# Kernel tuning notes

Hardware: AMD Instinct MI355X
Metric: run time of the kernel (lower is better)

## Reference

```python
import jax, jax.numpy as jnp
import numpy as np

B, S, H, T = 32, 1024, 1024, 256
WINDOW = 2
ITERATIONS = 3


def setup_inputs() -> dict:
    key = jax.random.key(0)
    k1, k2, k3, k4, k5, k6 = jax.random.split(key, 6)
    token_feats = jax.random.normal(k1, (B, S, H), dtype=jnp.float32)
    unary_score = jax.random.normal(k2, (B, S, T), dtype=jnp.float32)
    lengths = jax.random.randint(k3, (B,), S // 2, S + 1)  # in [S/2, S]
    mask = (jnp.arange(S)[None, :] < lengths[:, None]).astype(jnp.float32)
    transitions = jax.random.normal(k4, (WINDOW, T, T), dtype=jnp.float32)
    start_transitions = jax.random.normal(k5, (WINDOW, T), dtype=jnp.float32)
    end_transitions = jax.random.normal(k6, (WINDOW, T), dtype=jnp.float32)
    return {
        "token_feats": token_feats,
        "unary_score": unary_score,
        "mask": mask,
        "transitions": transitions,
        "start_transitions": start_transitions,
        "end_transitions": end_transitions,
        "lengths": lengths,
    }


def reference(token_feats, unary_score, mask, transitions, start_transitions,
              end_transitions, lengths):
    # mask unary (and token_feats, as in original; token_feats is unused in
    # the plain-transitions second-order path)
    unary = unary_score * mask[..., None]        # [B,S,T]
    _ = token_feats * mask[..., None]
    q = unary
    batch_range = jnp.arange(q.shape[0])
    for _it in range(ITERATIONS):
        q = jax.nn.softmax(q, axis=-1)
        left_sum = jnp.zeros_like(q)
        right_sum = jnp.zeros_like(q)
        for j in range(1, WINDOW + 1):
            # message from left neighbor at distance j
            left_sum = left_sum.at[:, j:].add(
                jnp.einsum('nsa,ab->nsb', q[:, :-j], transitions[j - 1]))
            # message from right neighbor at distance j
            right_sum = right_sum.at[:, :-j].add(
                jnp.einsum('nsb,ab->nsa', q[:, j:], transitions[j - 1]))
            # end transitions scatter-add at position lengths - j
            right_sum = right_sum.at[batch_range, lengths - j].add(
                end_transitions[j - 1])
        msg = left_sum + right_sum
        # start transitions on first WINDOW positions (broadcast over batch)
        msg = msg.at[:, 0:WINDOW].add(start_transitions)
        q = unary + msg
        q = q * mask[..., None]
    return q
```

## Files before the change

### kernel.cpp

```cpp
#include <hip/hip_runtime.h>
#include <hip/hip_bf16.h>
#include <cstdint>


typedef __attribute__((ext_vector_type(4))) float f32x4;
typedef __attribute__((ext_vector_type(8))) short bf16x8;

__device__ __forceinline__ void load_lds16(const void* g, void* l) {
    __builtin_amdgcn_global_load_lds(
        (const __attribute__((address_space(1))) void*)g,
        (__attribute__((address_space(3))) void*)l, 16, 0, 0);
}

__device__ __forceinline__ void wct_one(const float* __restrict__ trans,
                                        __hip_bfloat16* __restrict__ wct, int e) {
    int n = e >> 10, k = e & 1023;
    int r = k >> 8, kk = k & 255;
    float v;
    if (r == 0)      v = trans[kk * 256 + n];
    else if (r == 1) v = trans[65536 + kk * 256 + n];
    else if (r == 2) v = trans[n * 256 + kk];
    else             v = trans[65536 + n * 256 + kk];
    wct[n * 1024 + k] = __float2bfloat16(v);
}

__device__ __forceinline__ void guard_one(__hip_bfloat16* Pa, __hip_bfloat16* Pb, int g) {
    __hip_bfloat16* P = (g & 32768) ? Pb : Pa;
    int rem = g & 32767;
    int b = rem >> 10, wr = (rem >> 8) & 3, col = rem & 255;
    int row = b * 1028 + ((wr < 2) ? wr : 1024 + wr);
    P[row * 256 + col] = __float2bfloat16(0.f);
}

__device__ __forceinline__ void softmax0_row(const float* __restrict__ unary,
                                             const int* __restrict__ lengths,
                                             __hip_bfloat16* __restrict__ Pa,
                                             int row, int lane) {
    int b = row >> 10, s = row & 1023;
    float mval = (s < lengths[b]) ? 1.f : 0.f;
    float4 x = *((const float4*)(unary + (size_t)row * 256 + lane * 4));
    x.x *= mval; x.y *= mval; x.z *= mval; x.w *= mval;
    float mx = fmaxf(fmaxf(x.x, x.y), fmaxf(x.z, x.w));
    #pragma unroll
    for (int o = 32; o; o >>= 1) mx = fmaxf(mx, __shfl_xor(mx, o));
    float ea = __expf(x.x - mx), eb = __expf(x.y - mx);
    float ec = __expf(x.z - mx), ed = __expf(x.w - mx);
    float sum = ea + eb + ec + ed;
    #pragma unroll
    for (int o = 32; o; o >>= 1) sum += __shfl_xor(sum, o);
    float inv = 1.0f / sum;
    union { ushort4 u; __hip_bfloat16 h[4]; } o4;
    o4.h[0] = __float2bfloat16(ea * inv);
    o4.h[1] = __float2bfloat16(eb * inv);
    o4.h[2] = __float2bfloat16(ec * inv);
    o4.h[3] = __float2bfloat16(ed * inv);
    *((ushort4*)(Pa + ((size_t)b * 1028 + 2 + s) * 256 + lane * 4)) = o4.u;
}

__global__ __launch_bounds__(256) void prep_softmax0(
    const float* __restrict__ unary, const float* __restrict__ trans,
    const int* __restrict__ lengths,
    __hip_bfloat16* __restrict__ Pa, __hip_bfloat16* __restrict__ Pb,
    __hip_bfloat16* __restrict__ WcT)
{
    int tid = threadIdx.x, lane = tid & 63, wid = tid >> 6;
    int blk = blockIdx.x;
    int e0 = (blk * 256 + tid) * 2;
    wct_one(trans, WcT, e0);
    wct_one(trans, WcT, e0 + 1);
    int idx = blk * 256 + tid;
    if (idx < 65536) guard_one(Pa, Pb, idx);
    for (int q = 0; q < 16; ++q)
        softmax0_row(unary, lengths, Pa, blk * 64 + wid * 16 + q, lane);
}

__global__ __launch_bounds__(512, 4) void mfvi_iter_k(
    const __hip_bfloat16* __restrict__ Pin,
    const __hip_bfloat16* __restrict__ WcT,
    const float* __restrict__ unary, const int* __restrict__ lengths,
    const float* __restrict__ startT, const float* __restrict__ endT,
    __hip_bfloat16* __restrict__ Pout, float* __restrict__ out, int final_it)
{
    __shared__ __hip_bfloat16 Ps[68 * 128];
    __shared__ __hip_bfloat16 Bs[256 * 64];
    __shared__ float redA[256];
    __shared__ float redB[256];

    int tid = threadIdx.x;
    int lane = tid & 63, w = tid >> 6;
    int cn = lane & 15, quad = lane >> 4;
    int wm = (w >> 2) * 32, wn = (w & 3) * 64;
    int nslice = w & 3;
    int tile = blockIdx.x;
    int b = tile >> 4, s0 = (tile & 15) << 6;
    int len = lengths[b];
    const char* Pbase = (const char*)(Pin + ((size_t)b * 1028 + s0) * 256);

    f32x4 acc[2][4] = {};

    int sr = tid >> 3, sc = tid & 7;

    for (int h = 0; h < 2; ++h) {
        #pragma unroll
        for (int t = 0; t < 3; ++t) {
            int c = t * 512 + tid;
            if (t < 2 || tid < 64) {
                int row = c >> 4, ch = c & 15;
                int gch = (ch & ~7) | ((ch ^ row) & 7);
                load_lds16(Pbase + row * 512 + h * 256 + gch * 16,
                           (char*)Ps + c * 16);
            }
        }
        for (int p = 0; p < 8; ++p) {
            int region = p >> 1;
            int delta = (region == 0) ? -1 : (region == 1) ? -2
                      : (region == 2) ?  1 : 2;
            int k0 = region * 256 + h * 128 + (p & 1) * 64;

            #pragma unroll
            for (int c = 0; c < 4; ++c) {
                int n = c * 64 + sr;
                load_lds16((const char*)(WcT + n * 1024 + k0) + ((sc ^ (n & 7)) << 4),
                           (char*)Bs + c * 8192 + tid * 16);
            }
            __syncthreads();

            #pragma unroll
            for (int kk = 0; kk < 2; ++kk) {
                bf16x8 af[2], bfv[4];
                int gcb = (p & 1) * 8 + kk * 4 + quad;
                #pragma unroll
                for (int i = 0; i < 2; ++i) {
                    int r = wm + (i << 4) + cn + delta + 2;
                    int slot = (gcb & ~7) | ((gcb ^ r) & 7);
                    af[i] = *(const bf16x8*)((const char*)Ps + r * 256 + slot * 16);
                }
                int qb = kk * 4 + quad;
                #pragma unroll
                for (int j = 0; j < 4; ++j) {
                    int n = wn + (j << 4) + cn;
                    bfv[j] = *(const bf16x8*)((char*)Bs + n * 128 + ((qb ^ (n & 7)) << 4));
                }
                #pragma unroll
                for (int i = 0; i < 2; ++i)
                    #pragma unroll
                    for (int j = 0; j < 4; ++j)
                        acc[i][j] = __builtin_amdgcn_mfma_f32_16x16x32_bf16(
                            af[i], bfv[j], acc[i][j], 0, 0, 0);
            }
            __syncthreads();
        }
    }

    #pragma unroll
    for (int i = 0; i < 2; ++i)
        #pragma unroll
        for (int j = 0; j < 4; ++j) {
            int n = wn + (j << 4) + cn;
            #pragma unroll
            for (int r = 0; r < 4; ++r) {
                int s = s0 + wm + (i << 4) + (quad << 2) + r;
                float x = acc[i][j][r];
                if (s == 0)       x += startT[n];
                if (s == 1)       x += startT[256 + n];
                if (s == len - 1) x += endT[n];
                if (s == len - 2) x += endT[256 + n];
                long idx = ((long)((b << 10) + s)) * 256 + n;
                x += unary[idx];
                acc[i][j][r] = (s < len) ? x : 0.f;
            }
        }

    if (final_it) {
        #pragma unroll
        for (int i = 0; i < 2; ++i)
            #pragma unroll
            for (int j = 0; j < 4; ++j) {
                int n = wn + (j << 4) + cn;
                #pragma unroll
                for (int r = 0; r < 4; ++r) {
                    int s = s0 + wm + (i << 4) + (quad << 2) + r;
                    out[((long)((b << 10) + s)) * 256 + n] = acc[i][j][r];
                }
            }
        return;
    }

    #pragma unroll
    for (int i = 0; i < 2; ++i)
        #pragma unroll
        for (int r = 0; r < 4; ++r) {
            float m4 = fmaxf(fmaxf(acc[i][0][r], acc[i][1][r]),
                             fmaxf(acc[i][2][r], acc[i][3][r]));
            m4 = fmaxf(m4, __shfl_xor(m4, 1));
            m4 = fmaxf(m4, __shfl_xor(m4, 2));
            m4 = fmaxf(m4, __shfl_xor(m4, 4));
            m4 = fmaxf(m4, __shfl_xor(m4, 8));
            if (cn == 0)
                redA[(nslice << 6) + wm + (i << 4) + (quad << 2) + r] = m4;
        }
    __syncthreads();
    float M[2][4];
    #pragma unroll
    for (int i = 0; i < 2; ++i)
        #pragma unroll
        for (int r = 0; r < 4; ++r) {
            int row = wm + (i << 4) + (quad << 2) + r;
            M[i][r] = fmaxf(fmaxf(redA[row], redA[64 + row]),
                            fmaxf(redA[128 + row], redA[192 + row]));
        }
    #pragma unroll
    for (int i = 0; i < 2; ++i)
        #pragma unroll
        for (int r = 0; r < 4; ++r) {
            float s4 = 0.f;
            #pragma unroll
            for (int j = 0; j < 4; ++j) {
                float e = __expf(acc[i][j][r] - M[i][r]);
                acc[i][j][r] = e;
                s4 += e;
            }
            s4 += __shfl_xor(s4, 1);
            s4 += __shfl_xor(s4, 2);
            s4 += __shfl_xor(s4, 4);
            s4 += __shfl_xor(s4, 8);
            if (cn == 0)
                redB[(nslice << 6) + wm + (i << 4) + (quad << 2) + r] = s4;
        }
    __syncthreads();
    #pragma unroll
    for (int i = 0; i < 2; ++i)
        #pragma unroll
        for (int r = 0; r < 4; ++r) {
            int row = wm + (i << 4) + (quad << 2) + r;
            float inv = 1.0f / (redB[row] + redB[64 + row] +
                                redB[128 + row] + redB[192 + row]);
            int s = s0 + row;
            #pragma unroll
            for (int j = 0; j < 4; ++j) {
                int n = wn + (j << 4) + cn;
                Pout[((size_t)b * 1028 + 2 + s) * 256 + n] =
                    __float2bfloat16(acc[i][j][r] * inv);
            }
        }
}

extern "C" void kernel_launch(void* const* d_in, const int* in_sizes, int n_in,
                              void* d_out, int out_size, void* d_ws, size_t ws_size,
                              hipStream_t stream) {
    const float* unary  = (const float*)d_in[1];
    const float* trans  = (const float*)d_in[3];
    const float* startT = (const float*)d_in[4];
    const float* endT   = (const float*)d_in[5];
    const int*   lens   = (const int*)d_in[6];

    char* ws = (char*)d_ws;
    __hip_bfloat16* Pa  = (__hip_bfloat16*)ws;
    __hip_bfloat16* Pb  = (__hip_bfloat16*)(ws + ((size_t)32 << 20));
    __hip_bfloat16* WcT = (__hip_bfloat16*)(ws + ((size_t)64 << 20));
    float* out = (float*)d_out;

    prep_softmax0<<<dim3(512), dim3(256), 0, stream>>>(unary, trans, lens, Pa, Pb, WcT);
    mfvi_iter_k<<<dim3(512), dim3(512), 0, stream>>>(Pa, WcT, unary, lens, startT, endT, Pb, nullptr, 0);
    mfvi_iter_k<<<dim3(512), dim3(512), 0, stream>>>(Pb, WcT, unary, lens, startT, endT, Pa, nullptr, 0);
    mfvi_iter_k<<<dim3(512), dim3(512), 0, stream>>>(Pa, WcT, unary, lens, startT, endT, nullptr, out, 1);
}
```

Baseline: 287.9 us.

## Double-buffer weight tiles and load full P tile once into LDS

Loads the whole 68x256 bf16 P tile into shared memory once instead of in two halves, and restructures the K loop into 32 steps of 32-wide K chunks. Weight chunks are double-buffered so the next chunk's global-to-LDS load overlaps MFMA compute on the current one, with one barrier per step instead of two. The trade-off is more LDS per block, which may limit occupancy, and a new swizzle pattern for the smaller B chunks.

```diff
diff --git a/kernel.cpp b/kernel.cpp
--- a/kernel.cpp
+++ b/kernel.cpp
@@ -81,8 +81,8 @@
     const float* __restrict__ startT, const float* __restrict__ endT,
     __hip_bfloat16* __restrict__ Pout, float* __restrict__ out, int final_it)
 {
-    __shared__ __hip_bfloat16 Ps[68 * 128];
-    __shared__ __hip_bfloat16 Bs[256 * 64];
+    __shared__ __hip_bfloat16 Ps[68 * 256];
+    __shared__ __hip_bfloat16 Bs[2 * 256 * 32];
     __shared__ float redA[256];
     __shared__ float redB[256];
 
@@ -98,58 +98,61 @@
 
     f32x4 acc[2][4] = {};
 
-    int sr = tid >> 3, sc = tid & 7;
-
-    for (int h = 0; h < 2; ++h) {
-        #pragma unroll
-        for (int t = 0; t < 3; ++t) {
-            int c = t * 512 + tid;
-            if (t < 2 || tid < 64) {
-                int row = c >> 4, ch = c & 15;
-                int gch = (ch & ~7) | ((ch ^ row) & 7);
-                load_lds16(Pbase + row * 512 + h * 256 + gch * 16,
-                           (char*)Ps + c * 16);
-            }
-        }
-        for (int p = 0; p < 8; ++p) {
-            int region = p >> 1;
-            int delta = (region == 0) ? -1 : (region == 1) ? -2
-                      : (region == 2) ?  1 : 2;
-            int k0 = region * 256 + h * 128 + (p & 1) * 64;
-
-            #pragma unroll
-            for (int c = 0; c < 4; ++c) {
-                int n = c * 64 + sr;
-                load_lds16((const char*)(WcT + n * 1024 + k0) + ((sc ^ (n & 7)) << 4),
-                           (char*)Bs + c * 8192 + tid * 16);
-            }
-            __syncthreads();
-
-            #pragma unroll
-            for (int kk = 0; kk < 2; ++kk) {
-                bf16x8 af[2], bfv[4];
-                int gcb = (p & 1) * 8 + kk * 4 + quad;
-                #pragma unroll
-                for (int i = 0; i < 2; ++i) {
-                    int r = wm + (i << 4) + cn + delta + 2;
-                    int slot = (gcb & ~7) | ((gcb ^ r) & 7);
-                    af[i] = *(const bf16x8*)((const char*)Ps + r * 256 + slot * 16);
-                }
-                int qb = kk * 4 + quad;
-                #pragma unroll
-                for (int j = 0; j < 4; ++j) {
-                    int n = wn + (j << 4) + cn;
-                    bfv[j] = *(const bf16x8*)((char*)Bs + n * 128 + ((qb ^ (n & 7)) << 4));
-                }
-                #pragma unroll
-                for (int i = 0; i < 2; ++i)
-                    #pragma unroll
-                    for (int j = 0; j < 4; ++j)
-                        acc[i][j] = __builtin_amdgcn_mfma_f32_16x16x32_bf16(
-                            af[i], bfv[j], acc[i][j], 0, 0, 0);
-            }
-            __syncthreads();
-        }
+    #pragma unroll
+    for (int t = 0; t < 5; ++t) {
+        int c = t * 512 + tid;
+        if (t < 4 || tid < 128) {
+            int row = c >> 5, ch = c & 31;
+            int gch = (ch & ~7) | ((ch ^ row) & 7);
+            load_lds16(Pbase + row * 512 + gch * 16, (char*)Ps + c * 16);
+        }
+    }
+
+    auto stageB = [&](int bb, int p) {
+        int koff = p * 64;
+        #pragma unroll
+        for (int c = 0; c < 2; ++c) {
+            int sl = c * 512 + tid;
+            int n = sl >> 2, cs = sl & 3;
+            int g = cs ^ ((n >> 1) & 3);
+            load_lds16((const char*)WcT + n * 2048 + koff + g * 16,
+                       (char*)Bs + bb * 16384 + sl * 16);
+        }
+    };
+
+    stageB(0, 0);
+    __syncthreads();
+
+    #pragma unroll 2
+    for (int p = 0; p < 32; ++p) {
+        if (p < 31) stageB((p + 1) & 1, p + 1);
+
+        int region = p >> 3;
+        int delta = (region == 0) ? -1 : (region == 1) ? -2
+                  : (region == 2) ?  1 : 2;
+        int gcb = (p & 7) * 4 + quad;
+
+        bf16x8 af[2], bfv[4];
+        #pragma unroll
+        for (int i = 0; i < 2; ++i) {
+            int r = wm + (i << 4) + cn + delta + 2;
+            int slot = (gcb & ~7) | ((gcb ^ r) & 7);
+            af[i] = *(const bf16x8*)((const char*)Ps + r * 512 + slot * 16);
+        }
+        #pragma unroll
+        for (int j = 0; j < 4; ++j) {
+            int n = wn + (j << 4) + cn;
+            int cs = quad ^ ((n >> 1) & 3);
+            bfv[j] = *(const bf16x8*)((const char*)Bs + (p & 1) * 16384 + n * 64 + cs * 16);
+        }
+        #pragma unroll
+        for (int i = 0; i < 2; ++i)
+            #pragma unroll
+            for (int j = 0; j < 4; ++j)
+                acc[i][j] = __builtin_amdgcn_mfma_f32_16x16x32_bf16(
+                    af[i], bfv[j], acc[i][j], 0, 0, 0);
+
+        __syncthreads();
     }
 
     #pragma unroll
```

New measurement: 298.1 us. 3.6% more time.
